# Optimization experiments

Hardware: AMD Instinct MI355X
Metric: run time of the kernel (lower is better)

Reference implementation:

```python
import jax, jax.numpy as jnp
import numpy as np

B, S, H = 2, 2048, 2304
NH, HD, NKV = 8, 256, 4
WINDOW = 512
CAP = 50.0
THETA = 10000.0
NEG_INF = -2.3819763e38


def setup_inputs() -> dict:
    key = jax.random.key(0)
    ks = jax.random.split(key, 6)
    hidden_states = jax.random.normal(ks[0], (B, S, H), dtype=jnp.float32)
    # causal additive mask (0 where attend, -inf-ish where masked)
    i = jnp.arange(S)
    causal = i[None, :] <= i[:, None]
    attention_mask = jnp.broadcast_to(
        jnp.where(causal, 0.0, NEG_INF).astype(jnp.float32)[None, None], (B, 1, S, S)
    )
    position_ids = jnp.broadcast_to(jnp.arange(S, dtype=jnp.int32)[None], (B, S))
    scale = 0.02
    Wq = jax.random.normal(ks[1], (H, NH * HD), dtype=jnp.float32) * scale
    Wk = jax.random.normal(ks[2], (H, NKV * HD), dtype=jnp.float32) * scale
    Wv = jax.random.normal(ks[3], (H, NKV * HD), dtype=jnp.float32) * scale
    Wo = jax.random.normal(ks[4], (NH * HD, H), dtype=jnp.float32) * scale
    return {
        "hidden_states": hidden_states,
        "attention_mask": attention_mask,
        "position_ids": position_ids,
        "Wq": Wq,
        "Wk": Wk,
        "Wv": Wv,
        "Wo": Wo,
    }


def _rotate_half(x):
    h = x.shape[-1] // 2
    return jnp.concatenate([-x[..., h:], x[..., :h]], axis=-1)


def reference(hidden_states, attention_mask, position_ids, Wq, Wk, Wv, Wo):
    b, s, _ = hidden_states.shape
    q = (hidden_states @ Wq).reshape(b, s, NH, HD).transpose(0, 2, 1, 3)   # [B,NH,S,HD]
    k = (hidden_states @ Wk).reshape(b, s, NKV, HD).transpose(0, 2, 1, 3)  # [B,NKV,S,HD]
    v = (hidden_states @ Wv).reshape(b, s, NKV, HD).transpose(0, 2, 1, 3)
    # rotary embedding
    inv_freq = 1.0 / (THETA ** (jnp.arange(0, HD, 2, dtype=jnp.float32) / HD))
    freqs = position_ids.astype(jnp.float32)[..., None] * inv_freq  # [B,S,HD/2]
    emb = jnp.concatenate([freqs, freqs], axis=-1)                  # [B,S,HD]
    cos = jnp.cos(emb)[:, None]  # unsqueeze head dim
    sin = jnp.sin(emb)[:, None]
    q = q * cos + _rotate_half(q) * sin
    k = k * cos + _rotate_half(k) * sin
    # GQA: repeat kv heads
    rep = NH // NKV
    k = jnp.repeat(k, rep, axis=1)
    v = jnp.repeat(v, rep, axis=1)
    logits = jnp.einsum("bhqd,bhkd->bhqk", q, k) / jnp.sqrt(jnp.float32(HD))
    # sliding-window mask: keep |i-j| <= WINDOW-1, else NEG_INF
    idx = jnp.arange(s)
    sliding = jnp.abs(idx[:, None] - idx[None, :]) <= (WINDOW - 1)
    mask = jnp.where(sliding[None, None], attention_mask, NEG_INF)
    # tanh logit softcapping, then additive mask
    logits = jnp.tanh(logits / CAP) * CAP + mask
    probs = jax.nn.softmax(logits.astype(jnp.float32), axis=-1).astype(q.dtype)
    out = jnp.einsum("bhqk,bhkd->bhqd", probs, v)
    out = out.transpose(0, 2, 1, 3).reshape(b, s, NH * HD)
    return out @ Wo
```

## Files before the change

### kernel.cpp

```cpp
#include <hip/hip_runtime.h>
#include <cmath>

#define B_   2
#define S_   2048
#define H_   2304
#define NH_  8
#define HD_  256
#define NKV_ 4
#define WIN_ 512
#define QKVW 4096

typedef unsigned short ushort_t;
typedef __attribute__((ext_vector_type(8))) short bf16x8;
typedef __attribute__((ext_vector_type(4))) float floatx4;

__device__ __forceinline__ unsigned short f2bf(float f) {
  unsigned u = __builtin_bit_cast(unsigned, f);
  u += 0x7fff + ((u >> 16) & 1);
  return (unsigned short)(u >> 16);
}
__device__ __forceinline__ float bf2f(ushort_t v) {
  unsigned u = (unsigned)v << 16;
  return __builtin_bit_cast(float, u);
}

__device__ __forceinline__ void gl2lds16(const void* g, void* l) {
  __builtin_amdgcn_global_load_lds(
      (const __attribute__((address_space(1))) unsigned int*)g,
      (__attribute__((address_space(3))) unsigned int*)l, 16, 0, 0);
}

__global__ void cast_bf16(const float* __restrict__ in, ushort_t* __restrict__ out) {
  const int i = blockIdx.x * 256 + threadIdx.x;
  float4 v = ((const float4*)in)[i];
  ushort4 o;
  o.x = f2bf(v.x); o.y = f2bf(v.y); o.z = f2bf(v.z); o.w = f2bf(v.w);
  ((ushort4*)out)[i] = o;
}

__global__ void transpose_cast(const float* __restrict__ W, ushort_t* __restrict__ Wt,
                               int K, int N) {
  __shared__ float t[32][33];
  const int lx = threadIdx.x & 31, ly = threadIdx.x >> 5;
  const int n0 = blockIdx.x * 32, k0 = blockIdx.y * 32;
#pragma unroll
  for (int i = 0; i < 4; ++i)
    t[ly + i * 8][lx] = W[(long long)(k0 + ly + i * 8) * N + n0 + lx];
  __syncthreads();
#pragma unroll
  for (int i = 0; i < 4; ++i)
    Wt[(long long)(n0 + ly + i * 8) * K + k0 + lx] = f2bf(t[lx][ly + i * 8]);
}

#define RA(base_, qm_) do { \
  _Pragma("unroll") for (int i_ = 0; i_ < 4; ++i_) { \
    const int row_ = wm + (qm_) * 64 + i_ * 16 + l15; \
    _Pragma("unroll") for (int kk_ = 0; kk_ < 2; ++kk_) \
      a[i_][kk_] = *(const bf16x8*)&(base_)[row_ * 64 + (((kk_ * 4 + lq) ^ (l15 & 7)) * 8)]; \
  } \
} while (0)

#define RB(base_, qn_) do { \
  _Pragma("unroll") for (int j_ = 0; j_ < 2; ++j_) { \
    const int row_ = wn + (qn_) * 32 + j_ * 16 + l15; \
    _Pragma("unroll") for (int kk_ = 0; kk_ < 2; ++kk_) \
      b[j_][kk_] = *(const bf16x8*)&(base_)[row_ * 64 + (((kk_ * 4 + lq) ^ (l15 & 7)) * 8)]; \
  } \
} while (0)

#define MFMAQ(qm_, qn_) do { \
  __builtin_amdgcn_s_setprio(1); \
  _Pragma("unroll") for (int kk_ = 0; kk_ < 2; ++kk_) \
  _Pragma("unroll") for (int i_ = 0; i_ < 4; ++i_) \
  _Pragma("unroll") for (int j_ = 0; j_ < 2; ++j_) \
    acc[(qm_) * 4 + i_][(qn_) * 2 + j_] = __builtin_amdgcn_mfma_f32_16x16x32_bf16( \
        a[i_][kk_], b[j_][kk_], acc[(qm_) * 4 + i_][(qn_) * 2 + j_], 0, 0, 0); \
  __builtin_amdgcn_s_setprio(0); \
} while (0)

#define STAGE_A(dst_, gsrc_, t_, qm_) do { \
  _Pragma("unroll") for (int jj_ = 0; jj_ < 2; ++jj_) { \
    const int g_ = w * 2 + jj_; \
    const int tr0_ = ((g_ >> 3) * 128) + (qm_) * 64 + (g_ & 7) * 8; \
    gl2lds16(gsrc_ + (size_t)tr0_ * K + (size_t)(t_) * 64 + laneOff, dst_ + tr0_ * 64); \
  } \
} while (0)

#define STAGE_B(dst_, gsrc_, t_, qn_) do { \
  _Pragma("unroll") for (int jj_ = 0; jj_ < 2; ++jj_) { \
    const int g_ = w * 2 + jj_; \
    const int tr0_ = ((g_ >> 2) * 64) + (qn_) * 32 + (g_ & 3) * 8; \
    gl2lds16(gsrc_ + (size_t)tr0_ * K + (size_t)(t_) * 64 + laneOff, dst_ + tr0_ * 64); \
  } \
} while (0)

#define SB0()   __builtin_amdgcn_sched_barrier(0)
#define BARR()  do { SB0(); __builtin_amdgcn_s_barrier(); } while (0)
#define LGKM0() do { asm volatile("s_waitcnt lgkmcnt(0)" ::: "memory"); SB0(); } while (0)
#define LGKM8() asm volatile("s_waitcnt lgkmcnt(8)" ::: "memory")
#define VM(n_)  asm volatile("s_waitcnt vmcnt(" #n_ ")" ::: "memory")

template <bool OUT_BF16>
__launch_bounds__(512)
__global__ void gemm_8ph(const ushort_t* __restrict__ A,
                         const ushort_t* __restrict__ Bt,
                         void* __restrict__ Cv, int M, int N, int K) {
  extern __shared__ __attribute__((aligned(128))) ushort_t smem[];
  const int tid = threadIdx.x, lane = tid & 63, w = tid >> 6;
  const int wm = (w >> 2) * 128, wn = (w & 3) * 64;
  const int l15 = lane & 15, lq = lane >> 4;

  const int nwg  = gridDim.x * gridDim.y;
  const int orig = blockIdx.y * gridDim.x + blockIdx.x;
  const int cpx  = nwg >> 3;
  const int swz  = (orig & 7) * cpx + (orig >> 3);
  const int bx   = swz % gridDim.x, by = swz / gridDim.x;
  const int bm = by * 256, bn = bx * 256;
  const int NT = K >> 6;

  const ushort_t* Ab = A + (size_t)bm * K;
  const ushort_t* Bb = Bt + (size_t)bn * K;
  const size_t laneOff = (size_t)(lane >> 3) * K + (size_t)(((lane & 7) ^ (lane >> 3)) * 8);

  ushort_t* Ae = smem;
  ushort_t* Ao = smem + 16384;
  ushort_t* Be = smem + 32768;
  ushort_t* Bo = smem + 49152;

  floatx4 acc[8][4] = {};
  bf16x8 a[4][2], b[2][2];

  STAGE_A(Ae, Ab, 0, 0);
  STAGE_B(Be, Bb, 0, 1);
  STAGE_A(Ae, Ab, 0, 1);
  STAGE_B(Be, Bb, 0, 0);
  STAGE_A(Ao, Ab, 1, 0);
  STAGE_B(Bo, Bb, 1, 1);
  VM(4);
  BARR();

  for (int t = 0; t < NT; t += 2) {
    const bool more = (t + 2 < NT);

    RA(Ae, 0); RB(Be, 0);
    STAGE_A(Ao, Ab, t + 1, 1);
    LGKM8();
    BARR();
    LGKM0();
    MFMAQ(0, 0);
    BARR();

    RB(Be, 1);
    STAGE_B(Bo, Bb, t + 1, 0);
    BARR();
    LGKM0();
    MFMAQ(0, 1);
    BARR();

    RA(Ae, 1);
    if (more) STAGE_A(Ae, Ab, t + 2, 0);
    BARR();
    LGKM0();
    MFMAQ(1, 1);
    BARR();

    RB(Be, 0);
    if (more) STAGE_B(Be, Bb, t + 2, 1);
    BARR();
    LGKM0();
    MFMAQ(1, 0);
    SB0();
    if (more) { VM(4); } else { VM(0); }
    BARR();

    RA(Ao, 0); RB(Bo, 0);
    if (more) STAGE_A(Ae, Ab, t + 2, 1);
    LGKM8();
    BARR();
    LGKM0();
    MFMAQ(0, 0);
    BARR();

    RB(Bo, 1);
    if (more) STAGE_B(Be, Bb, t + 2, 0);
    BARR();
    LGKM0();
    MFMAQ(0, 1);
    BARR();

    RA(Ao, 1);
    if (more) STAGE_A(Ao, Ab, t + 3, 0);
    BARR();
    LGKM0();
    MFMAQ(1, 1);
    BARR();

    RB(Bo, 0);
    if (more) STAGE_B(Bo, Bb, t + 3, 1);
    BARR();
    LGKM0();
    MFMAQ(1, 0);
    SB0();
    if (more) { VM(4); } else { VM(0); }
    BARR();
  }

  const int r0 = lq * 4;
#pragma unroll
  for (int mf = 0; mf < 8; ++mf)
#pragma unroll
    for (int nf = 0; nf < 4; ++nf) {
      const long long base = (long long)(bm + wm + mf * 16 + r0) * N + bn + wn + nf * 16 + l15;
      if (OUT_BF16) {
        ushort_t* Cp = (ushort_t*)Cv + base;
#pragma unroll
        for (int rr = 0; rr < 4; ++rr) Cp[(long long)rr * N] = f2bf(acc[mf][nf][rr]);
      } else {
        float* Cp = (float*)Cv + base;
#pragma unroll
        for (int rr = 0; rr < 4; ++rr) Cp[(long long)rr * N] = acc[mf][nf][rr];
      }
    }
}

#undef RA
#undef RB
#undef MFMAQ
#undef STAGE_A
#undef STAGE_B
#undef SB0
#undef BARR
#undef LGKM0
#undef LGKM8
#undef VM

template <bool OUT_BF16>
__launch_bounds__(256)
__global__ void gemm_bt(const ushort_t* __restrict__ A,
                        const ushort_t* __restrict__ Bt,
                        void* __restrict__ Cv, int M, int N, int K) {
  __shared__ ushort_t As[128 * 64];
  __shared__ ushort_t Bs[128 * 64];
  const int tid = threadIdx.x, lane = tid & 63, wid = tid >> 6;
  const int bm = blockIdx.y * 128, bn = blockIdx.x * 128;
  const int wm = (wid >> 1) * 64, wn = (wid & 1) * 64;

  floatx4 acc[4][4] = {};

  const int r  = tid >> 1;
  const int cp = (tid & 1) * 4;
  const int wkey = r & 7;
  const ushort_t* Ap = A  + (long long)(bm + r) * K + cp * 8;
  const ushort_t* Bp = Bt + (long long)(bn + r) * K + cp * 8;
  ushort_t* Aw = &As[r * 64];
  ushort_t* Bw = &Bs[r * 64];

  const int l15 = lane & 15, lq = lane >> 4;
  const int rkey = l15 & 7;

  bf16x8 ar[4], br[4];
#pragma unroll
  for (int i = 0; i < 4; ++i) {
    ar[i] = *(const bf16x8*)(Ap + i * 8);
    br[i] = *(const bf16x8*)(Bp + i * 8);
  }

  for (int k0 = 0; k0 < K; k0 += 64) {
    __syncthreads();
#pragma unroll
    for (int i = 0; i < 4; ++i) {
      *(bf16x8*)&Aw[((cp + i) ^ wkey) * 8] = ar[i];
      *(bf16x8*)&Bw[((cp + i) ^ wkey) * 8] = br[i];
    }
    __syncthreads();

    if (k0 + 64 < K) {
      const int kn = k0 + 64;
#pragma unroll
      for (int i = 0; i < 4; ++i) {
        ar[i] = *(const bf16x8*)(Ap + kn + i * 8);
        br[i] = *(const bf16x8*)(Bp + kn + i * 8);
      }
    }

#pragma unroll
    for (int kk = 0; kk < 2; ++kk) {
      bf16x8 af[4], bfr[4];
#pragma unroll
      for (int i = 0; i < 4; ++i) {
        af[i]  = *(const bf16x8*)&As[(wm + i * 16 + l15) * 64 + ((kk * 4 + lq) ^ rkey) * 8];
        bfr[i] = *(const bf16x8*)&Bs[(wn + i * 16 + l15) * 64 + ((kk * 4 + lq) ^ rkey) * 8];
      }
#pragma unroll
      for (int i = 0; i < 4; ++i)
#pragma unroll
        for (int j = 0; j < 4; ++j)
          acc[i][j] = __builtin_amdgcn_mfma_f32_16x16x32_bf16(af[i], bfr[j], acc[i][j], 0, 0, 0);
    }
  }

  const int r0 = lq * 4, c0 = l15;
#pragma unroll
  for (int i = 0; i < 4; ++i)
#pragma unroll
    for (int j = 0; j < 4; ++j) {
      const long long base = (long long)(bm + wm + i * 16 + r0) * N + bn + wn + j * 16 + c0;
      if (OUT_BF16) {
        ushort_t* Cp = (ushort_t*)Cv + base;
#pragma unroll
        for (int rr = 0; rr < 4; ++rr) Cp[(long long)rr * N] = f2bf(acc[i][j][rr]);
      } else {
        float* Cp = (float*)Cv + base;
#pragma unroll
        for (int rr = 0; rr < 4; ++rr) Cp[(long long)rr * N] = acc[i][j][rr];
      }
    }
}

__global__ void rope_inplace(ushort_t* __restrict__ QKV16, const int* __restrict__ pos) {
  const int bs  = blockIdx.x;
  const int gid = blockIdx.y * 256 + threadIdx.x;
  const int head = gid >> 7;
  const int d    = gid & 127;
  const float pp   = (float)pos[bs];
  const float invf = __expf(-(float)d * (9.210340371976184f / 128.0f));
  const float ang  = pp * invf;
  float sn, cc;
  __sincosf(ang, &sn, &cc);
  ushort_t* base = QKV16 + (size_t)bs * QKVW + head * HD_;
  const float x1 = bf2f(base[d]);
  const float x2 = bf2f(base[d + 128]);
  float o1 = x1 * cc - x2 * sn;
  float o2 = x2 * cc + x1 * sn;
  if (head < NH_) { o1 *= 0.0625f; o2 *= 0.0625f; }
  base[d]       = f2bf(o1);
  base[d + 128] = f2bf(o2);
}

__global__ void v_prep(const ushort_t* __restrict__ QKV16, ushort_t* __restrict__ Vt16) {
  __shared__ ushort_t tile[32][33];
  const int k0 = blockIdx.x * 32, d0 = blockIdx.y * 32;
  const int b = blockIdx.z >> 2, hk = blockIdx.z & 3;
  const int lx = threadIdx.x & 31, ly = threadIdx.x >> 5;
#pragma unroll
  for (int i = 0; i < 4; ++i)
    tile[ly + 8 * i][lx] =
        QKV16[(size_t)(b * S_ + k0 + ly + 8 * i) * QKVW + 3072 + hk * HD_ + d0 + lx];
  __syncthreads();
#pragma unroll
  for (int i = 0; i < 4; ++i)
    Vt16[((size_t)(b * NKV_ + hk) * HD_ + d0 + ly + 8 * i) * S_ + k0 + lx] =
        tile[lx][ly + 8 * i];
}

__launch_bounds__(512)
__global__ void attn_mfma(const ushort_t* __restrict__ QKV16,
                          const ushort_t* __restrict__ Vt16,
                          ushort_t* __restrict__ AOb) {
  __shared__ ushort_t Ks[32 * 256];
  __shared__ ushort_t Vts[256 * 32];
  __shared__ ushort_t Ps[8][16 * 32];
  __shared__ float rsb[8][16];

  const int lane = threadIdx.x & 63, w = threadIdx.x >> 6;
  const int l15 = lane & 15, lq = lane >> 4;
  const int qb = blockIdx.x * 64;
  const int hp = blockIdx.y, b = blockIdx.z;
  const int h  = hp * 2 + (w >> 2);
  const int hw = w & 3;

  const ushort_t* Qh = QKV16 + (size_t)b * S_ * QKVW + h * HD_;
  const ushort_t* Kh = QKV16 + (size_t)b * S_ * QKVW + 2048 + hp * HD_;
  const ushort_t* Vh = Vt16 + ((size_t)(b * NKV_ + hp) * HD_) * S_;

  const int qw = qb + hw * 16;

  bf16x8 afq[8];
  {
    const ushort_t* qr = Qh + (size_t)(qw + l15) * QKVW + lq * 8;
#pragma unroll
    for (int kd = 0; kd < 8; ++kd) afq[kd] = *(const bf16x8*)(qr + kd * 32);
  }

  floatx4 acc[16] = {};
  float rs[4] = {0.f, 0.f, 0.f, 0.f};

  int kb0 = qb - (WIN_ - 1);
  if (kb0 < 0) kb0 = 0;
  kb0 &= ~31;

  const int ksp = lane & 31, ksr = lane >> 5;
  const int vsp = lane & 3,  vsr = lane >> 2;

  for (int kb = kb0; kb < qb + 64; kb += 32) {
    __syncthreads();
#pragma unroll
    for (int i = 0; i < 2; ++i) {
      const int kl = w * 4 + 2 * i + ksr;
      gl2lds16(Kh + (size_t)(kb + kl) * QKVW + (ksp ^ (kl & 31)) * 8,
               &Ks[(w * 4 + 2 * i) * 256]);
    }
#pragma unroll
    for (int i = 0; i < 2; ++i) {
      const int dl = w * 32 + 16 * i + vsr;
      gl2lds16(Vh + (size_t)dl * S_ + kb + (vsp ^ ((dl >> 1) & 3)) * 8,
               &Vts[(w * 32 + 16 * i) * 32]);
    }
    __syncthreads();

    if (kb <= qw + 15 && kb + 31 >= qw - (WIN_ - 1)) {
      ushort_t* Pw = Ps[w];
#pragma unroll
      for (int kt = 0; kt < 2; ++kt) {
        floatx4 sacc = {};
        const int keyl = kt * 16 + l15;
        const int krow = keyl * 256;
        const int ksw = keyl & 31;
#pragma unroll
        for (int kd = 0; kd < 8; ++kd) {
          bf16x8 bk = *(const bf16x8*)&Ks[krow + ((kd * 4 + lq) ^ ksw) * 8];
          sacc = __builtin_amdgcn_mfma_f32_16x16x32_bf16(afq[kd], bk, sacc, 0, 0, 0);
        }
        const int keyg = kb + keyl;
#pragma unroll
        for (int rr = 0; rr < 4; ++rr) {
          const int qg = qw + lq * 4 + rr;
          const float t = __expf(sacc[rr] * 0.04f);
          const float L = 50.f - __fdividef(100.f, t + 1.f);
          float p = __expf(L);
          p = (keyg <= qg && keyg >= qg - (WIN_ - 1)) ? p : 0.f;
          rs[rr] += p;
          const int ql = lq * 4 + rr;
          const int ch = kt * 2 + (l15 >> 3);
          Pw[ql * 32 + ((ch ^ ((ql >> 1) & 3)) * 8) + (l15 & 7)] = f2bf(p);
        }
      }
      asm volatile("s_waitcnt lgkmcnt(0)" ::: "memory");

      const bf16x8 bp = *(const bf16x8*)&Pw[l15 * 32 + ((lq ^ ((l15 >> 1) & 3)) * 8)];
      const int vsw = (l15 >> 1) & 3;
#pragma unroll
      for (int t = 0; t < 16; ++t) {
        bf16x8 av = *(const bf16x8*)&Vts[(t * 16 + l15) * 32 + ((lq ^ vsw) * 8)];
        acc[t] = __builtin_amdgcn_mfma_f32_16x16x32_bf16(av, bp, acc[t], 0, 0, 0);
      }
    }
  }

#pragma unroll
  for (int rr = 0; rr < 4; ++rr) {
    rs[rr] += __shfl_xor(rs[rr], 1, 64);
    rs[rr] += __shfl_xor(rs[rr], 2, 64);
    rs[rr] += __shfl_xor(rs[rr], 4, 64);
    rs[rr] += __shfl_xor(rs[rr], 8, 64);
  }
  if (l15 == 0) {
#pragma unroll
    for (int rr = 0; rr < 4; ++rr) rsb[w][lq * 4 + rr] = rs[rr];
  }
  asm volatile("s_waitcnt lgkmcnt(0)" ::: "memory");
  __builtin_amdgcn_wave_barrier();
  const float inv = 1.0f / rsb[w][l15];

  const size_t ob = ((size_t)(b * S_ + qw + l15) * NH_ + h) * HD_;
#pragma unroll
  for (int t = 0; t < 16; ++t) {
    ushort4 o;
    o.x = f2bf(acc[t][0] * inv);
    o.y = f2bf(acc[t][1] * inv);
    o.z = f2bf(acc[t][2] * inv);
    o.w = f2bf(acc[t][3] * inv);
    *(ushort4*)&AOb[ob + t * 16 + lq * 4] = o;
  }
}

extern "C" void kernel_launch(void* const* d_in, const int* in_sizes, int n_in,
                              void* d_out, int out_size, void* d_ws, size_t ws_size,
                              hipStream_t stream) {
  const float* X   = (const float*)d_in[0];
  const int*   pos = (const int*)d_in[2];
  const float* Wq  = (const float*)d_in[3];
  const float* Wk  = (const float*)d_in[4];
  const float* Wv  = (const float*)d_in[5];
  const float* Wo  = (const float*)d_in[6];
  float* out = (float*)d_out;

  const int M  = B_ * S_;
  const int NQ = NH_ * HD_;
  const int NK = NKV_ * HD_;

  char* w = (char*)d_ws;
  ushort_t* QKV16 = (ushort_t*)w;  w += (size_t)M * QKVW * 2;
  ushort_t* Xb    = (ushort_t*)w;  w += (size_t)M * H_ * 2;
  ushort_t* Wqkvt = (ushort_t*)w;  w += (size_t)QKVW * H_ * 2;
  ushort_t* Wot   = (ushort_t*)w;  w += (size_t)H_ * NQ * 2;
  ushort_t* Vt16  = (ushort_t*)w;  w += (size_t)B_ * NKV_ * S_ * HD_ * 2;
  ushort_t* AOb   = (ushort_t*)w;  w += (size_t)M * NQ * 2;

  static bool g_init = false, g_8ph_ok = false;
  if (!g_init) {
    hipError_t e1 = hipFuncSetAttribute(
        reinterpret_cast<const void*>(&gemm_8ph<true>),
        hipFuncAttributeMaxDynamicSharedMemorySize, 131072);
    g_8ph_ok = (e1 == hipSuccess);
    g_init = true;
  }

  dim3 blk(256);

  cast_bf16<<<(M * H_) / 1024, blk, 0, stream>>>(X, Xb);
  transpose_cast<<<dim3(NQ / 32, H_ / 32), blk, 0, stream>>>(Wq, Wqkvt, H_, NQ);
  transpose_cast<<<dim3(NK / 32, H_ / 32), blk, 0, stream>>>(Wk, Wqkvt + (size_t)2048 * H_, H_, NK);
  transpose_cast<<<dim3(NK / 32, H_ / 32), blk, 0, stream>>>(Wv, Wqkvt + (size_t)3072 * H_, H_, NK);
  transpose_cast<<<dim3(H_ / 32, NQ / 32), blk, 0, stream>>>(Wo, Wot, NQ, H_);

  if (g_8ph_ok) {
    gemm_8ph<true><<<dim3(QKVW / 256, M / 256), dim3(512), 131072, stream>>>(
        Xb, Wqkvt, QKV16, M, QKVW, H_);
  } else {
    gemm_bt<true><<<dim3(QKVW / 128, M / 128), blk, 0, stream>>>(Xb, Wqkvt, QKV16, M, QKVW, H_);
  }

  rope_inplace<<<dim3(M, 6), blk, 0, stream>>>(QKV16, pos);
  v_prep<<<dim3(S_ / 32, HD_ / 32, B_ * NKV_), blk, 0, stream>>>(QKV16, Vt16);

  attn_mfma<<<dim3(S_ / 64, NKV_, B_), dim3(512), 0, stream>>>(QKV16, Vt16, AOb);

  gemm_bt<false><<<dim3(H_ / 128, M / 128), blk, 0, stream>>>(AOb, Wot, out, M, H_, NQ);
}
```

Baseline: 361.0 us.

## Double-buffer K/V tiles in attention kernel and raise MFMA priority

The attention kernel now keeps two LDS buffers for K and V tiles and issues the global-to-LDS copy of the next tile before computing on the current one. This aims to hide load latency and removes one barrier per iteration. It also wraps the MFMA loops in s_setprio so matrix work gets issue priority. The cost is roughly double the LDS per block, which may lower occupancy, and a static-LDS fallback kernel is kept in case the dynamic-LDS attribute cannot be set.

```diff
diff --git a/kernel.cpp b/kernel.cpp
--- a/kernel.cpp
+++ b/kernel.cpp
@@ -353,14 +353,69 @@
         tile[lx][ly + 8 * i];
 }
 
+#define ATTN_STG_KV(KD_, VD_, kb_) do { \
+  _Pragma("unroll") for (int i_ = 0; i_ < 2; ++i_) { \
+    const int kl_ = w * 4 + 2 * i_ + ksr; \
+    gl2lds16(Kh + (size_t)((kb_) + kl_) * QKVW + (ksp ^ (kl_ & 31)) * 8, \
+             (KD_) + (w * 4 + 2 * i_) * 256); \
+  } \
+  _Pragma("unroll") for (int i_ = 0; i_ < 2; ++i_) { \
+    const int dl_ = w * 32 + 16 * i_ + vsr; \
+    gl2lds16(Vh + (size_t)dl_ * S_ + (kb_) + (vsp ^ ((dl_ >> 1) & 3)) * 8, \
+             (VD_) + (w * 32 + 16 * i_) * 32); \
+  } \
+} while (0)
+
+#define ATTN_BODY(Kc_, Vc_) do { \
+  if (kb <= qw + 15 && kb + 31 >= qw - (WIN_ - 1)) { \
+    ushort_t* Pw = PsA + w * 512; \
+    _Pragma("unroll") for (int kt = 0; kt < 2; ++kt) { \
+      floatx4 sacc = {}; \
+      const int keyl = kt * 16 + l15; \
+      const int krow = keyl * 256; \
+      const int ksw = keyl & 31; \
+      __builtin_amdgcn_s_setprio(1); \
+      _Pragma("unroll") for (int kd = 0; kd < 8; ++kd) { \
+        bf16x8 bk = *(const bf16x8*)&(Kc_)[krow + ((kd * 4 + lq) ^ ksw) * 8]; \
+        sacc = __builtin_amdgcn_mfma_f32_16x16x32_bf16(afq[kd], bk, sacc, 0, 0, 0); \
+      } \
+      __builtin_amdgcn_s_setprio(0); \
+      const int keyg = kb + keyl; \
+      _Pragma("unroll") for (int rr = 0; rr < 4; ++rr) { \
+        const int qg = qw + lq * 4 + rr; \
+        const float t = __expf(sacc[rr] * 0.04f); \
+        const float L = 50.f - __fdividef(100.f, t + 1.f); \
+        float p = __expf(L); \
+        p = (keyg <= qg && keyg >= qg - (WIN_ - 1)) ? p : 0.f; \
+        rs[rr] += p; \
+        const int ql = lq * 4 + rr; \
+        const int ch = kt * 2 + (l15 >> 3); \
+        Pw[ql * 32 + ((ch ^ ((ql >> 1) & 3)) * 8) + (l15 & 7)] = f2bf(p); \
+      } \
+    } \
+    asm volatile("s_waitcnt lgkmcnt(0)" ::: "memory"); \
+    const bf16x8 bp = *(const bf16x8*)&Pw[l15 * 32 + ((lq ^ ((l15 >> 1) & 3)) * 8)]; \
+    const int vsw = (l15 >> 1) & 3; \
+    __builtin_amdgcn_s_setprio(1); \
+    _Pragma("unroll") for (int tt = 0; tt < 16; ++tt) { \
+      bf16x8 av = *(const bf16x8*)&(Vc_)[(tt * 16 + l15) * 32 + ((lq ^ vsw) * 8)]; \
+      acc[tt] = __builtin_amdgcn_mfma_f32_16x16x32_bf16(av, bp, acc[tt], 0, 0, 0); \
+    } \
+    __builtin_amdgcn_s_setprio(0); \
+  } \
+} while (0)
+
 __launch_bounds__(512)
 __global__ void attn_mfma(const ushort_t* __restrict__ QKV16,
                           const ushort_t* __restrict__ Vt16,
                           ushort_t* __restrict__ AOb) {
-  __shared__ ushort_t Ks[32 * 256];
-  __shared__ ushort_t Vts[256 * 32];
-  __shared__ ushort_t Ps[8][16 * 32];
-  __shared__ float rsb[8][16];
+  extern __shared__ __attribute__((aligned(128))) ushort_t alds[];
+  ushort_t* Ks0 = alds;
+  ushort_t* Ks1 = alds + 8192;
+  ushort_t* Vt0 = alds + 16384;
+  ushort_t* Vt1 = alds + 24576;
+  ushort_t* PsA = alds + 32768;
+  float*    rsb = (float*)(alds + 32768 + 4096);
 
   const int lane = threadIdx.x & 63, w = threadIdx.x >> 6;
   const int l15 = lane & 15, lq = lane >> 4;
@@ -388,63 +443,24 @@
   int kb0 = qb - (WIN_ - 1);
   if (kb0 < 0) kb0 = 0;
   kb0 &= ~31;
+  const int kbEnd = qb + 64;
 
   const int ksp = lane & 31, ksr = lane >> 5;
   const int vsp = lane & 3,  vsr = lane >> 2;
 
-  for (int kb = kb0; kb < qb + 64; kb += 32) {
+  ATTN_STG_KV(Ks0, Vt0, kb0);
+  __syncthreads();
+
+  int tog = 0;
+  for (int kb = kb0; kb < kbEnd; kb += 32) {
+    ushort_t* Kc = tog ? Ks1 : Ks0;
+    ushort_t* Vc = tog ? Vt1 : Vt0;
+    ushort_t* Kn = tog ? Ks0 : Ks1;
+    ushort_t* Vn = tog ? Vt0 : Vt1;
+    if (kb + 32 < kbEnd) ATTN_STG_KV(Kn, Vn, kb + 32);
+    ATTN_BODY(Kc, Vc);
     __syncthreads();
-#pragma unroll
-    for (int i = 0; i < 2; ++i) {
-      const int kl = w * 4 + 2 * i + ksr;
-      gl2lds16(Kh + (size_t)(kb + kl) * QKVW + (ksp ^ (kl & 31)) * 8,
-               &Ks[(w * 4 + 2 * i) * 256]);
-    }
-#pragma unroll
-    for (int i = 0; i < 2; ++i) {
-      const int dl = w * 32 + 16 * i + vsr;
-      gl2lds16(Vh + (size_t)dl * S_ + kb + (vsp ^ ((dl >> 1) & 3)) * 8,
-               &Vts[(w * 32 + 16 * i) * 32]);
-    }
-    __syncthreads();
-
-    if (kb <= qw + 15 && kb + 31 >= qw - (WIN_ - 1)) {
-      ushort_t* Pw = Ps[w];
-#pragma unroll
-      for (int kt = 0; kt < 2; ++kt) {
-        floatx4 sacc = {};
-        const int keyl = kt * 16 + l15;
-        const int krow = keyl * 256;
-        const int ksw = keyl & 31;
-#pragma unroll
-        for (int kd = 0; kd < 8; ++kd) {
-          bf16x8 bk = *(const bf16x8*)&Ks[krow + ((kd * 4 + lq) ^ ksw) * 8];
-          sacc = __builtin_amdgcn_mfma_f32_16x16x32_bf16(afq[kd], bk, sacc, 0, 0, 0);
-        }
-        const int keyg = kb + keyl;
-#pragma unroll
-        for (int rr = 0; rr < 4; ++rr) {
-          const int qg = qw + lq * 4 + rr;
-          const float t = __expf(sacc[rr] * 0.04f);
-          const float L = 50.f - __fdividef(100.f, t + 1.f);
-          float p = __expf(L);
-          p = (keyg <= qg && keyg >= qg - (WIN_ - 1)) ? p : 0.f;
-          rs[rr] += p;
-          const int ql = lq * 4 + rr;
-          const int ch = kt * 2 + (l15 >> 3);
-          Pw[ql * 32 + ((ch ^ ((ql >> 1) & 3)) * 8) + (l15 & 7)] = f2bf(p);
-        }
-      }
-      asm volatile("s_waitcnt lgkmcnt(0)" ::: "memory");
-
-      const bf16x8 bp = *(const bf16x8*)&Pw[l15 * 32 + ((lq ^ ((l15 >> 1) & 3)) * 8)];
-      const int vsw = (l15 >> 1) & 3;
-#pragma unroll
-      for (int t = 0; t < 16; ++t) {
-        bf16x8 av = *(const bf16x8*)&Vts[(t * 16 + l15) * 32 + ((lq ^ vsw) * 8)];
-        acc[t] = __builtin_amdgcn_mfma_f32_16x16x32_bf16(av, bp, acc[t], 0, 0, 0);
-      }
-    }
+    tog ^= 1;
   }
 
 #pragma unroll
@@ -456,11 +472,11 @@
   }
   if (l15 == 0) {
 #pragma unroll
-    for (int rr = 0; rr < 4; ++rr) rsb[w][lq * 4 + rr] = rs[rr];
+    for (int rr = 0; rr < 4; ++rr) rsb[w * 16 + lq * 4 + rr] = rs[rr];
   }
   asm volatile("s_waitcnt lgkmcnt(0)" ::: "memory");
   __builtin_amdgcn_wave_barrier();
-  const float inv = 1.0f / rsb[w][l15];
+  const float inv = 1.0f / rsb[w * 16 + l15];
 
   const size_t ob = ((size_t)(b * S_ + qw + l15) * NH_ + h) * HD_;
 #pragma unroll
@@ -473,6 +489,83 @@
     *(ushort4*)&AOb[ob + t * 16 + lq * 4] = o;
   }
 }
+
+__launch_bounds__(512)
+__global__ void attn_mfma_s(const ushort_t* __restrict__ QKV16,
+                            const ushort_t* __restrict__ Vt16,
+                            ushort_t* __restrict__ AOb) {
+  __shared__ ushort_t Ks[32 * 256];
+  __shared__ ushort_t Vts[256 * 32];
+  __shared__ ushort_t PsS[8][16 * 32];
+  __shared__ float rsbS[8][16];
+
+  const int lane = threadIdx.x & 63, w = threadIdx.x >> 6;
+  const int l15 = lane & 15, lq = lane >> 4;
+  const int qb = blockIdx.x * 64;
+  const int hp = blockIdx.y, b = blockIdx.z;
+  const int h  = hp * 2 + (w >> 2);
+  const int hw = w & 3;
+
+  const ushort_t* Qh = QKV16 + (size_t)b * S_ * QKVW + h * HD_;
+  const ushort_t* Kh = QKV16 + (size_t)b * S_ * QKVW + 2048 + hp * HD_;
+  const ushort_t* Vh = Vt16 + ((size_t)(b * NKV_ + hp) * HD_) * S_;
+
+  const int qw = qb + hw * 16;
+
+  bf16x8 afq[8];
+  {
+    const ushort_t* qr = Qh + (size_t)(qw + l15) * QKVW + lq * 8;
+#pragma unroll
+    for (int kd = 0; kd < 8; ++kd) afq[kd] = *(const bf16x8*)(qr + kd * 32);
+  }
+
+  floatx4 acc[16] = {};
+  float rs[4] = {0.f, 0.f, 0.f, 0.f};
+
+  int kb0 = qb - (WIN_ - 1);
+  if (kb0 < 0) kb0 = 0;
+  kb0 &= ~31;
+
+  const int ksp = lane & 31, ksr = lane >> 5;
+  const int vsp = lane & 3,  vsr = lane >> 2;
+
+  for (int kb = kb0; kb < qb + 64; kb += 32) {
+    __syncthreads();
+    ATTN_STG_KV(Ks, Vts, kb);
+    __syncthreads();
+    ushort_t* PsA = &PsS[0][0];
+    ATTN_BODY(Ks, Vts);
+  }
+
+#pragma unroll
+  for (int rr = 0; rr < 4; ++rr) {
+    rs[rr] += __shfl_xor(rs[rr], 1, 64);
+    rs[rr] += __shfl_xor(rs[rr], 2, 64);
+    rs[rr] += __shfl_xor(rs[rr], 4, 64);
+    rs[rr] += __shfl_xor(rs[rr], 8, 64);
+  }
+  if (l15 == 0) {
+#pragma unroll
+    for (int rr = 0; rr < 4; ++rr) rsbS[w][lq * 4 + rr] = rs[rr];
+  }
+  asm volatile("s_waitcnt lgkmcnt(0)" ::: "memory");
+  __builtin_amdgcn_wave_barrier();
+  const float inv = 1.0f / rsbS[w][l15];
+
+  const size_t ob = ((size_t)(b * S_ + qw + l15) * NH_ + h) * HD_;
+#pragma unroll
+  for (int t = 0; t < 16; ++t) {
+    ushort4 o;
+    o.x = f2bf(acc[t][0] * inv);
+    o.y = f2bf(acc[t][1] * inv);
+    o.z = f2bf(acc[t][2] * inv);
+    o.w = f2bf(acc[t][3] * inv);
+    *(ushort4*)&AOb[ob + t * 16 + lq * 4] = o;
+  }
+}
+
+#undef ATTN_STG_KV
+#undef ATTN_BODY
 
 extern "C" void kernel_launch(void* const* d_in, const int* in_sizes, int n_in,
                               void* d_out, int out_size, void* d_ws, size_t ws_size,
@@ -497,12 +590,16 @@
   ushort_t* Vt16  = (ushort_t*)w;  w += (size_t)B_ * NKV_ * S_ * HD_ * 2;
   ushort_t* AOb   = (ushort_t*)w;  w += (size_t)M * NQ * 2;
 
-  static bool g_init = false, g_8ph_ok = false;
+  static bool g_init = false, g_8ph_ok = false, g_attn_ok = false;
   if (!g_init) {
     hipError_t e1 = hipFuncSetAttribute(
         reinterpret_cast<const void*>(&gemm_8ph<true>),
         hipFuncAttributeMaxDynamicSharedMemorySize, 131072);
     g_8ph_ok = (e1 == hipSuccess);
+    hipError_t e2 = hipFuncSetAttribute(
+        reinterpret_cast<const void*>(&attn_mfma),
+        hipFuncAttributeMaxDynamicSharedMemorySize, 74240);
+    g_attn_ok = (e2 == hipSuccess);
     g_init = true;
   }
 
@@ -524,7 +621,11 @@
   rope_inplace<<<dim3(M, 6), blk, 0, stream>>>(QKV16, pos);
   v_prep<<<dim3(S_ / 32, HD_ / 32, B_ * NKV_), blk, 0, stream>>>(QKV16, Vt16);
 
-  attn_mfma<<<dim3(S_ / 64, NKV_, B_), dim3(512), 0, stream>>>(QKV16, Vt16, AOb);
+  if (g_attn_ok) {
+    attn_mfma<<<dim3(S_ / 64, NKV_, B_), dim3(512), 74240, stream>>>(QKV16, Vt16, AOb);
+  } else {
+    attn_mfma_s<<<dim3(S_ / 64, NKV_, B_), dim3(512), 0, stream>>>(QKV16, Vt16, AOb);
+  }
 
   gemm_bt<false><<<dim3(H_ / 128, M / 128), blk, 0, stream>>>(AOb, Wot, out, M, H_, NQ);
 }
```

Measured after the change: 353.7 us. 2.0% less time.
